# Kernel tuning notes

Measured on AMD Instinct MI355X. Metric: run time of the kernel, lower is better.

Reference implementation:

```python
import jax, jax.numpy as jnp
import numpy as np

NB, CH, NY, NX, NC = 2, 64, 80, 80, 80
STRIDE = 4.0


def _conv(x, w, b, pad):
    y = jax.lax.conv_general_dilated(x, w, (1, 1), [(pad, pad), (pad, pad)],
                                     dimension_numbers=('NCHW', 'OIHW', 'NCHW'))
    return y + b[None, :, None, None]


def _head(x, w1, b1, w2, b2, final_relu):
    y = jax.nn.relu(_conv(x, w1, b1, 1))
    y = _conv(y, w2, b2, 0)
    return jax.nn.relu(y) if final_relu else y


def setup_inputs() -> dict:
    key = jax.random.key(0)
    ks = jax.random.split(key, 16)
    s = 0.05

    def cw(k, o, i, kk):
        return jax.random.normal(k, (o, i, kk, kk), jnp.float32) * s

    def cb(k, o):
        return jax.random.normal(k, (o,), jnp.float32) * s

    inp = {
        'x': jax.random.normal(ks[0], (NB, CH, NY, NX), jnp.float32),
        # offsets: [batch_index, off_x, off_y] per image (esod tile offsets)
        'offsets': jnp.concatenate([
            jnp.arange(NB, dtype=jnp.float32)[:, None],
            jax.random.uniform(ks[1], (NB, 2), jnp.float32) * 4.0], axis=1),
        'hm_w1': cw(ks[2], CH, CH, 3), 'hm_b1': cb(ks[3], CH),
        'hm_w2': cw(ks[4], NC, CH, 1), 'hm_b2': jnp.full((NC,), -2.19, jnp.float32),
        'wh_w1': cw(ks[5], CH, CH, 3), 'wh_b1': cb(ks[6], CH),
        'wh_w2': cw(ks[7], 2, CH, 1), 'wh_b2': cb(ks[8], 2),
        'reg_w1': cw(ks[9], CH, CH, 3), 'reg_b1': cb(ks[10], CH),
        'reg_w2': cw(ks[11], 2, CH, 1), 'reg_b2': cb(ks[12], 2),
    }
    return inp


def _forward(x, offsets, hm_w1, hm_b1, hm_w2, hm_b2,
             wh_w1, wh_b1, wh_w2, wh_b2,
             reg_w1, reg_b1, reg_w2, reg_b2):
    hm = _head(x, hm_w1, hm_b1, hm_w2, hm_b2, False)    # (nb, nc, ny, nx)
    wh = _head(x, wh_w1, wh_b1, wh_w2, wh_b2, True)     # (nb, 2, ny, nx)
    reg = _head(x, reg_w1, reg_b1, reg_w2, reg_b2, True)
    nb, nc, ny, nx = hm.shape

    wh_ = jnp.transpose(wh, (0, 2, 3, 1))   # (nb, ny, nx, 2)
    reg_ = jnp.transpose(reg, (0, 2, 3, 1))
    yv, xv = jnp.meshgrid(jnp.arange(ny), jnp.arange(nx), indexing='ij')
    grid = jnp.stack([xv, yv], -1).astype(jnp.float32)[None]  # (1, ny, nx, 2)

    off_xy = offsets[:, 1:3].reshape(nb, 1, 1, 2) * 2.0
    ctr = grid + off_xy + reg_
    bbox = jnp.concatenate([ctr - wh_ / 2.0, ctr + wh_ / 2.0], -1) * STRIDE  # xyxy

    # xyxy -> xywh (same per-image boxes for every class channel)
    cxy = (bbox[..., :2] + bbox[..., 2:]) / 2.0
    bwh = bbox[..., 2:] - bbox[..., :2]
    xywh = jnp.concatenate([cxy, bwh], -1)              # (nb, ny, nx, 4)

    hm_ = jax.nn.sigmoid(hm)
    hmax = jax.lax.reduce_window(hm_, -jnp.inf, jax.lax.max,
                                 (1, 1, 3, 3), (1, 1, 1, 1),
                                 [(0, 0), (0, 0), (1, 1), (1, 1)])
    maxima = (hmax == hm_)                              # (nb, nc, ny, nx)

    no = 5 + nc
    xywh_b = jnp.broadcast_to(xywh[:, None], (nb, nc, ny, nx, 4))
    score = hm_[..., None]
    oh = jnp.broadcast_to(jnp.eye(nc, dtype=hm_.dtype)[None, :, None, None, :],
                          (nb, nc, ny, nx, nc))
    rows = jnp.concatenate([xywh_b, score, oh], -1)     # (nb, nc, ny, nx, no)

    K = nc * ny * nx
    rows = rows.reshape(nb, K, no)
    m = maxima.reshape(nb, K)

    def compact(r, mk):
        # stable sort: maxima rows first, preserving (c, y, x) scan order
        order = jnp.argsort(jnp.logical_not(mk), stable=True)
        return r[order] * mk[order][:, None].astype(r.dtype)

    return jax.vmap(compact)(rows, m)                   # (nb, K, 5+nc), zero-padded


def reference(x, offsets, hm_w1, hm_b1, hm_w2, hm_b2,
              wh_w1, wh_b1, wh_w2, wh_b2,
              reg_w1, reg_b1, reg_w2, reg_b2):
    return _forward(x, offsets, hm_w1, hm_b1, hm_w2, hm_b2,
                    wh_w1, wh_b1, wh_w2, wh_b2,
                    reg_w1, reg_b1, reg_w2, reg_b2)
```

## Files before the change

kernel.cpp:

```cpp
#include <hip/hip_runtime.h>
#include <math.h>

#define NBATCH 2
#define CHN    64
#define NYY    80
#define NXX    80
#define NCLS   80
#define NPIX   6400
#define KTOT   512000
#define NOUT   85
#define NBLK   500

typedef float vf4 __attribute__((ext_vector_type(4)));

#define QTOT   21760000L
#define QF1    13056000L
#define QF2    16320000L

__global__ __launch_bounds__(320)
void conv1_kernel(const float* __restrict__ x,
                  const float* __restrict__ hw1, const float* __restrict__ hb1,
                  const float* __restrict__ ww1, const float* __restrict__ wb1,
                  const float* __restrict__ rw1, const float* __restrict__ rb1,
                  double* __restrict__ c1hm, float* __restrict__ c1wr,
                  vf4* __restrict__ outq)
{
    __shared__ double smem_d[4992];
    const int bl = blockIdx.x;
    const int t  = threadIdx.x;

    const int gtid = bl * 320 + t;
    const int nth  = 640 * 320;
    const vf4 fz = {0.f, 0.f, 0.f, 0.f};

    if (bl < 320) {
        float*  lxf = (float*)smem_d;
        double* lwd = (double*)((char*)smem_d + 21504);

        const int yt  = bl % 40;
        const int ocg = (bl / 40) % 4;
        const int b   = bl / 160;

        const int pxq = t % 80;
        const int ocq = t / 80;
        const int r   = pxq / 40;
        const int c   = (pxq % 40) * 2;
        const int oc0 = ocg * 16 + ocq * 4;
        const int gy0 = yt * 2;

        const float* xin = x + (size_t)b * CHN * NPIX;

        double acc[2][4];
        #pragma unroll
        for (int j = 0; j < 2; j++)
            #pragma unroll
            for (int o = 0; o < 4; o++) acc[j][o] = (double)hb1[oc0 + o];

        for (int cc = 0; cc < 4; cc++) {
            const int icc = cc * 16;
            __syncthreads();
            for (int j = t; j < 1280; j += 320) {
                int ic_l = j / 80; int rem = j % 80;
                int row_l = rem / 20; int c4 = (rem % 20) * 4;
                int gy = gy0 - 1 + row_l;
                float4 v = make_float4(0.f, 0.f, 0.f, 0.f);
                if ((unsigned)gy < 80u)
                    v = *(const float4*)(xin + (size_t)(icc + ic_l) * NPIX + gy * NXX + c4);
                float* dst = &lxf[(ic_l * 4 + row_l) * 84];
                dst[c4 + 1] = v.x; dst[c4 + 2] = v.y;
                dst[c4 + 3] = v.z; dst[c4 + 4] = v.w;
            }
            for (int j = t; j < 64; j += 320) {
                lxf[j * 84 + 0]  = 0.f;
                lxf[j * 84 + 81] = 0.f;
            }
            for (int j = t; j < 2304; j += 320) {
                int oc_l = j % 16; int k = j / 16;
                int ic_l = k / 9, tap = k % 9;
                lwd[k * 16 + oc_l] =
                    (double)hw1[((size_t)(ocg * 16 + oc_l) * CHN + icc + ic_l) * 9 + tap];
            }
            __syncthreads();
            {
                int i0 = cc * 16, i1 = i0 + 16;
                for (int i = i0; i < i1; i++) {
                    long q = (long)gtid + (long)i * nth;
                    if (q < QF1) __builtin_nontemporal_store(fz, outq + q);
                }
            }
            for (int ic = 0; ic < 16; ic++) {
                double xw[3][4];
                #pragma unroll
                for (int ky = 0; ky < 3; ky++) {
                    const float* row = &lxf[(ic * 4 + r + ky) * 84];
                    float2 a  = *(const float2*)&row[c];
                    float2 bb = *(const float2*)&row[c + 2];
                    xw[ky][0] = (double)a.x;  xw[ky][1] = (double)a.y;
                    xw[ky][2] = (double)bb.x; xw[ky][3] = (double)bb.y;
                }
                #pragma unroll
                for (int ky = 0; ky < 3; ky++)
                #pragma unroll
                for (int kx = 0; kx < 3; kx++) {
                    const double* wv = &lwd[(ic * 9 + ky * 3 + kx) * 16 + ocq * 4];
                    double w0 = wv[0], w1d = wv[1], w2 = wv[2], w3 = wv[3];
                    double x0 = xw[ky][kx], x1 = xw[ky][kx + 1];
                    acc[0][0] += x0 * w0; acc[0][1] += x0 * w1d;
                    acc[0][2] += x0 * w2; acc[0][3] += x0 * w3;
                    acc[1][0] += x1 * w0; acc[1][1] += x1 * w1d;
                    acc[1][2] += x1 * w2; acc[1][3] += x1 * w3;
                }
            }
        }
        size_t pix = (size_t)(gy0 + r) * NXX + c;
        #pragma unroll
        for (int o = 0; o < 4; o++) {
            double2 v;
            v.x = acc[0][o] > 0.0 ? acc[0][o] : 0.0;
            v.y = acc[1][o] > 0.0 ? acc[1][o] : 0.0;
            *(double2*)(c1hm + ((size_t)b * CHN + oc0 + o) * NPIX + pix) = v;
        }
    } else {
        float* lxw = (float*)smem_d;
        float* lwf = (float*)((char*)smem_d + 30720);

        const int blw = bl - 320;
        const int yt  = blw % 20;
        const int ocg = (blw / 20) % 4;
        const int img = blw / 80;

        const int head = img >> 1, b = img & 1;
        const float* w1 = (head == 0) ? ww1 : rw1;
        const float* b1 = (head == 0) ? wb1 : rb1;
        const float* xin = x + (size_t)b * CHN * NPIX;

        const int pxq = t % 80;
        const int ocq = t / 80;
        const int r   = pxq / 20;
        const int c   = (pxq % 20) * 4;
        const int oc0 = ocg * 16 + ocq * 4;
        const int gy0 = yt * 4;

        float acc[4][4];
        #pragma unroll
        for (int j = 0; j < 4; j++)
            #pragma unroll
            for (int o = 0; o < 4; o++) acc[j][o] = b1[oc0 + o];

        for (int cc = 0; cc < 4; cc++) {
            const int icc = cc * 16;
            __syncthreads();
            for (int j = t; j < 1920; j += 320) {
                int ic_l = j / 120; int rem = j % 120;
                int row_l = rem / 20; int c4 = (rem % 20) * 4;
                int gy = gy0 - 1 + row_l;
                float4 v = make_float4(0.f, 0.f, 0.f, 0.f);
                if ((unsigned)gy < 80u)
                    v = *(const float4*)(xin + (size_t)(icc + ic_l) * NPIX + gy * NXX + c4);
                *(float4*)&lxw[(ic_l * 6 + row_l) * 80 + c4] = v;
            }
            for (int j = t; j < 2304; j += 320) {
                int oc_l = j % 16; int k = j / 16;
                int ic_l = k / 9, tap = k % 9;
                lwf[k * 16 + oc_l] =
                    w1[((size_t)(ocg * 16 + oc_l) * CHN + icc + ic_l) * 9 + tap];
            }
            __syncthreads();
            {
                int i0 = cc * 16, i1 = i0 + 16;
                for (int i = i0; i < i1; i++) {
                    long q = (long)gtid + (long)i * nth;
                    if (q < QF1) __builtin_nontemporal_store(fz, outq + q);
                }
            }
            for (int ic = 0; ic < 16; ic++) {
                float xw[3][6];
                #pragma unroll
                for (int ky = 0; ky < 3; ky++) {
                    const float* row = &lxw[(ic * 6 + r + ky) * 80];
                    xw[ky][0] = (c > 0) ? row[c - 1] : 0.f;
                    float4 m = *(const float4*)&row[c];
                    xw[ky][1] = m.x; xw[ky][2] = m.y;
                    xw[ky][3] = m.z; xw[ky][4] = m.w;
                    xw[ky][5] = (c < 76) ? row[c + 4] : 0.f;
                }
                #pragma unroll
                for (int ky = 0; ky < 3; ky++)
                #pragma unroll
                for (int kx = 0; kx < 3; kx++) {
                    const float* wv = &lwf[(ic * 9 + ky * 3 + kx) * 16 + ocq * 4];
                    float w0 = wv[0], w1v = wv[1], w2 = wv[2], w3 = wv[3];
                    #pragma unroll
                    for (int j = 0; j < 4; j++) {
                        float xv = xw[ky][j + kx];
                        acc[j][0] += xv * w0; acc[j][1] += xv * w1v;
                        acc[j][2] += xv * w2; acc[j][3] += xv * w3;
                    }
                }
            }
        }
        size_t pix = (size_t)(gy0 + r) * NXX + c;
        #pragma unroll
        for (int o = 0; o < 4; o++) {
            float4 v;
            v.x = fmaxf(acc[0][o], 0.f); v.y = fmaxf(acc[1][o], 0.f);
            v.z = fmaxf(acc[2][o], 0.f); v.w = fmaxf(acc[3][o], 0.f);
            *(float4*)(c1wr + ((size_t)img * CHN + oc0 + o) * NPIX + pix) = v;
        }
    }
}

__global__ __launch_bounds__(256)
void conv2_hm_kernel(const double* __restrict__ c1,
                     const float* __restrict__ w2,
                     const float* __restrict__ b2,
                     double* __restrict__ hm_z,
                     vf4* __restrict__ outq)
{
    int p   = blockIdx.x * 256 + threadIdx.x;
    int oc0 = blockIdx.y * 4;
    int b   = blockIdx.z;

    {
        const int bl   = (blockIdx.z * 20 + blockIdx.y) * 25 + blockIdx.x;
        const int gtid = bl * 256 + threadIdx.x;
        const vf4 fz = {0.f, 0.f, 0.f, 0.f};
        for (int i = 0; i < 13; i++) {
            long q = QF1 + (long)gtid + (long)i * 256000;
            if (q < QF2) __builtin_nontemporal_store(fz, outq + q);
        }
    }

    const double* in = c1 + (size_t)b * CHN * NPIX;
    double acc[4];
    #pragma unroll
    for (int o = 0; o < 4; o++) acc[o] = (double)b2[oc0 + o];

    for (int ic = 0; ic < CHN; ic++) {
        double xv = in[(size_t)ic * NPIX + p];
        #pragma unroll
        for (int o = 0; o < 4; o++)
            acc[o] += xv * (double)w2[(size_t)(oc0 + o) * CHN + ic];
    }
    #pragma unroll
    for (int o = 0; o < 4; o++)
        hm_z[((size_t)b * NCLS + oc0 + o) * NPIX + p] = acc[o];
}

__global__ __launch_bounds__(256)
void conv2_wr_kernel(const float* __restrict__ c1,
                     const float* __restrict__ wh_w2, const float* __restrict__ wh_b2,
                     const float* __restrict__ rg_w2, const float* __restrict__ rg_b2,
                     float* __restrict__ wh, float* __restrict__ rg)
{
    int p  = blockIdx.x * 256 + threadIdx.x;
    int hc = blockIdx.y;
    int b  = blockIdx.z;
    int head = hc >> 1, ch = hc & 1;

    const float* in = c1 + ((size_t)(head * 2 + b) * CHN) * NPIX;
    const float* w  = (head == 0) ? wh_w2 + (size_t)ch * CHN : rg_w2 + (size_t)ch * CHN;
    float bias      = (head == 0) ? wh_b2[ch] : rg_b2[ch];

    float acc = bias;
    for (int ic = 0; ic < CHN; ic++) acc += in[(size_t)ic * NPIX + p] * w[ic];
    acc = fmaxf(acc, 0.f);
    float* o = (head == 0) ? wh : rg;
    o[((size_t)b * 2 + ch) * NPIX + p] = acc;
}

__global__ void flags_kernel(const double* __restrict__ hm_z,
                             unsigned long long* __restrict__ ballots,
                             unsigned int* __restrict__ counts,
                             vf4* __restrict__ outq)
{
    int b = blockIdx.y;
    int k = blockIdx.x * 1024 + threadIdx.x;

    {
        const int gtid = (b * NBLK + blockIdx.x) * 1024 + threadIdx.x;
        const vf4 fz = {0.f, 0.f, 0.f, 0.f};
        for (int i = 0; i < 6; i++) {
            long q = QF2 + (long)gtid + (long)i * 1024000;
            if (q < QTOT) __builtin_nontemporal_store(fz, outq + q);
        }
    }

    int c = k / NPIX;
    int p = k - c * NPIX;
    int y = p / NXX, xx = p - y * NXX;

    const double* h = hm_z + ((size_t)b * NCLS + c) * NPIX;
    double s = h[p];
    double m = s;
    #pragma unroll
    for (int dy = -1; dy <= 1; dy++) {
        int yy = y + dy;
        if ((unsigned)yy >= (unsigned)NYY) continue;
        const double* hr = h + yy * NXX;
        #pragma unroll
        for (int dx = -1; dx <= 1; dx++) {
            int xn = xx + dx;
            if ((unsigned)xn >= (unsigned)NXX) continue;
            double v = hr[xn];
            m = v > m ? v : m;
        }
    }
    bool flag = (s == m);
    unsigned long long ball = __ballot(flag);
    int lane = threadIdx.x & 63;
    int wave = threadIdx.x >> 6;

    __shared__ unsigned int wcnt[16];
    if (lane == 0) {
        ballots[(size_t)b * 8000 + blockIdx.x * 16 + wave] = ball;
        wcnt[wave] = __popcll(ball);
    }
    __syncthreads();
    if (threadIdx.x == 0) {
        unsigned int tot = 0;
        for (int i = 0; i < 16; i++) tot += wcnt[i];
        counts[b * NBLK + blockIdx.x] = tot;
    }
}

__global__ void scan_kernel(const unsigned int* __restrict__ counts,
                            unsigned int* __restrict__ offs)
{
    int b = blockIdx.x;
    int t = threadIdx.x;
    unsigned int v = (t < NBLK) ? counts[b * NBLK + t] : 0u;
    unsigned int xi = v;
    #pragma unroll
    for (int d = 1; d < 64; d <<= 1) {
        unsigned int n = __shfl_up(xi, d, 64);
        if ((t & 63) >= d) xi += n;
    }
    __shared__ unsigned int wtot[8];
    __shared__ unsigned int wbase[8];
    if ((t & 63) == 63) wtot[t >> 6] = xi;
    __syncthreads();
    if (t == 0) {
        unsigned int a = 0;
        for (int i = 0; i < 8; i++) { wbase[i] = a; a += wtot[i]; }
    }
    __syncthreads();
    unsigned int excl = xi - v + wbase[t >> 6];
    if (t < NBLK) offs[b * NBLK + t] = excl;
}

__global__ void scatter_kernel(const unsigned long long* __restrict__ ballots,
                               const unsigned int* __restrict__ offs,
                               const double* __restrict__ hm_z,
                               const float* __restrict__ wh,
                               const float* __restrict__ rg,
                               const float* __restrict__ offsets,
                               float* __restrict__ out)
{
    int b = blockIdx.y;
    int k = blockIdx.x * 1024 + threadIdx.x;
    int lane = threadIdx.x & 63;
    int wave = threadIdx.x >> 6;

    unsigned long long ball = ballots[(size_t)b * 8000 + blockIdx.x * 16 + wave];

    __shared__ unsigned int wc[16];
    __shared__ unsigned int wb[16];
    if (lane == 0) wc[wave] = __popcll(ball);
    __syncthreads();
    if (threadIdx.x == 0) {
        unsigned int a = 0;
        for (int i = 0; i < 16; i++) { wb[i] = a; a += wc[i]; }
    }
    __syncthreads();

    bool flag = (ball >> lane) & 1ull;
    if (!flag) return;

    unsigned int rank = offs[b * NBLK + blockIdx.x] + wb[wave]
                      + (unsigned int)__popcll(ball & ((1ull << lane) - 1ull));

    int c = k / NPIX;
    int p = k - c * NPIX;
    int y = p / NXX, xx = p - y * NXX;

    float offx = offsets[b * 3 + 1];
    float offy = offsets[b * 3 + 2];
    float r0 = rg[((size_t)b * 2 + 0) * NPIX + p];
    float r1 = rg[((size_t)b * 2 + 1) * NPIX + p];
    float w0 = wh[((size_t)b * 2 + 0) * NPIX + p];
    float w1 = wh[((size_t)b * 2 + 1) * NPIX + p];
    double z = hm_z[((size_t)b * NCLS + c) * NPIX + p];
    float s  = (float)(1.0 / (1.0 + exp(-z)));

    float cx = ((float)xx + 2.f * offx + r0) * 4.f;
    float cy = ((float)y  + 2.f * offy + r1) * 4.f;

    float* row = out + ((size_t)b * KTOT + rank) * NOUT;
    row[0] = cx;
    row[1] = cy;
    row[2] = w0 * 4.f;
    row[3] = w1 * 4.f;
    row[4] = s;
    row[5 + c] = 1.f;
}

extern "C" void kernel_launch(void* const* d_in, const int* in_sizes, int n_in,
                              void* d_out, int out_size, void* d_ws, size_t ws_size,
                              hipStream_t stream)
{
    const float* x       = (const float*)d_in[0];
    const float* offsets = (const float*)d_in[1];
    const float* hm_w1   = (const float*)d_in[2];
    const float* hm_b1   = (const float*)d_in[3];
    const float* hm_w2   = (const float*)d_in[4];
    const float* hm_b2   = (const float*)d_in[5];
    const float* wh_w1   = (const float*)d_in[6];
    const float* wh_b1   = (const float*)d_in[7];
    const float* wh_w2   = (const float*)d_in[8];
    const float* wh_b2   = (const float*)d_in[9];
    const float* reg_w1  = (const float*)d_in[10];
    const float* reg_b1  = (const float*)d_in[11];
    const float* reg_w2  = (const float*)d_in[12];
    const float* reg_b2  = (const float*)d_in[13];

    float* out = (float*)d_out;
    vf4* outq  = (vf4*)d_out;

    char* wp = (char*)d_ws;
    double* c1hm = (double*)wp;                 wp += (size_t)NBATCH * CHN * NPIX * 8;
    double* hm_z = (double*)wp;                 wp += (size_t)NBATCH * NCLS * NPIX * 8;
    float*  c1wr = (float*)wp;                  wp += (size_t)2 * NBATCH * CHN * NPIX * 4;
    float*  wh   = (float*)wp;                  wp += (size_t)NBATCH * 2 * NPIX * 4;
    float*  rg   = (float*)wp;                  wp += (size_t)NBATCH * 2 * NPIX * 4;
    unsigned long long* ballots = (unsigned long long*)wp; wp += (size_t)NBATCH * 8000 * 8;
    unsigned int* counts = (unsigned int*)wp;   wp += (size_t)NBATCH * NBLK * 4;
    unsigned int* offs   = (unsigned int*)wp;

    conv1_kernel<<<640, 320, 0, stream>>>(
        x, hm_w1, hm_b1, wh_w1, wh_b1, reg_w1, reg_b1, c1hm, c1wr, outq);

    conv2_hm_kernel<<<dim3(25, 20, 2), 256, 0, stream>>>(c1hm, hm_w2, hm_b2, hm_z, outq);

    conv2_wr_kernel<<<dim3(25, 4, 2), 256, 0, stream>>>(
        c1wr, wh_w2, wh_b2, reg_w2, reg_b2, wh, rg);

    flags_kernel<<<dim3(NBLK, 2), 1024, 0, stream>>>(hm_z, ballots, counts, outq);

    scan_kernel<<<2, 512, 0, stream>>>(counts, offs);

    scatter_kernel<<<dim3(NBLK, 2), 1024, 0, stream>>>(
        ballots, offs, hm_z, wh, rg, offsets, out);
}
```

Before: 154.4 us.

## Double conv1 grid with smaller per-block tiles and rebalance output zeroing across kernels

Splits conv1 work into twice as many blocks: the fp64 heatmap path now computes 8 output channels per block instead of 16, and the wh/reg path uses 2-row tiles with a padded shared layout matching the hm path. Shared memory per block shrinks, which can raise occupancy. The zero-fill of the output buffer is redistributed: flags_kernel now zeroes fewer chunks and scatter_kernel zeroes the final region. The intent is more parallelism for conv1 and spreading memset traffic, at the cost of more redundant input loads and scatter blocks that both zero and write output.

```diff
diff --git a/kernel.cpp b/kernel.cpp
--- a/kernel.cpp
+++ b/kernel.cpp
@@ -16,6 +16,7 @@
 #define QTOT   21760000L
 #define QF1    13056000L
 #define QF2    16320000L
+#define QF3    19584000L
 
 __global__ __launch_bounds__(320)
 void conv1_kernel(const float* __restrict__ x,
@@ -25,36 +26,37 @@
                   double* __restrict__ c1hm, float* __restrict__ c1wr,
                   vf4* __restrict__ outq)
 {
-    __shared__ double smem_d[4992];
+    __shared__ double smem_d[3840];
     const int bl = blockIdx.x;
     const int t  = threadIdx.x;
 
     const int gtid = bl * 320 + t;
-    const int nth  = 640 * 320;
+    const int nth  = 1280 * 320;
     const vf4 fz = {0.f, 0.f, 0.f, 0.f};
 
-    if (bl < 320) {
-        float*  lxf = (float*)smem_d;
+    const int pxq = t % 80;
+    const int ocq = t / 80;
+    const int r   = pxq / 40;
+    const int c   = (pxq % 40) * 2;
+
+    float* lxf = (float*)smem_d;
+
+    if (bl < 640) {
         double* lwd = (double*)((char*)smem_d + 21504);
 
         const int yt  = bl % 40;
-        const int ocg = (bl / 40) % 4;
-        const int b   = bl / 160;
-
-        const int pxq = t % 80;
-        const int ocq = t / 80;
-        const int r   = pxq / 40;
-        const int c   = (pxq % 40) * 2;
-        const int oc0 = ocg * 16 + ocq * 4;
+        const int ocg = (bl / 40) % 8;
+        const int b   = bl / 320;
+        const int oc0 = ocg * 8 + ocq * 2;
         const int gy0 = yt * 2;
 
         const float* xin = x + (size_t)b * CHN * NPIX;
 
-        double acc[2][4];
+        double acc[2][2];
         #pragma unroll
         for (int j = 0; j < 2; j++)
             #pragma unroll
-            for (int o = 0; o < 4; o++) acc[j][o] = (double)hb1[oc0 + o];
+            for (int o = 0; o < 2; o++) acc[j][o] = (double)hb1[oc0 + o];
 
         for (int cc = 0; cc < 4; cc++) {
             const int icc = cc * 16;
@@ -74,15 +76,15 @@
                 lxf[j * 84 + 0]  = 0.f;
                 lxf[j * 84 + 81] = 0.f;
             }
-            for (int j = t; j < 2304; j += 320) {
-                int oc_l = j % 16; int k = j / 16;
+            for (int j = t; j < 1152; j += 320) {
+                int oc_l = j % 8; int k = j / 8;
                 int ic_l = k / 9, tap = k % 9;
-                lwd[k * 16 + oc_l] =
-                    (double)hw1[((size_t)(ocg * 16 + oc_l) * CHN + icc + ic_l) * 9 + tap];
+                lwd[k * 8 + oc_l] =
+                    (double)hw1[((size_t)(ocg * 8 + oc_l) * CHN + icc + ic_l) * 9 + tap];
             }
             __syncthreads();
             {
-                int i0 = cc * 16, i1 = i0 + 16;
+                int i0 = cc * 8, i1 = i0 + 8;
                 for (int i = i0; i < i1; i++) {
                     long q = (long)gtid + (long)i * nth;
                     if (q < QF1) __builtin_nontemporal_store(fz, outq + q);
@@ -102,62 +104,61 @@
                 for (int ky = 0; ky < 3; ky++)
                 #pragma unroll
                 for (int kx = 0; kx < 3; kx++) {
-                    const double* wv = &lwd[(ic * 9 + ky * 3 + kx) * 16 + ocq * 4];
-                    double w0 = wv[0], w1d = wv[1], w2 = wv[2], w3 = wv[3];
+                    const double* wv = &lwd[(ic * 9 + ky * 3 + kx) * 8 + ocq * 2];
+                    double w0 = wv[0], w1d = wv[1];
                     double x0 = xw[ky][kx], x1 = xw[ky][kx + 1];
                     acc[0][0] += x0 * w0; acc[0][1] += x0 * w1d;
-                    acc[0][2] += x0 * w2; acc[0][3] += x0 * w3;
                     acc[1][0] += x1 * w0; acc[1][1] += x1 * w1d;
-                    acc[1][2] += x1 * w2; acc[1][3] += x1 * w3;
-                }
-            }
-        }
-        size_t pix = (size_t)(gy0 + r) * NXX + c;
-        #pragma unroll
-        for (int o = 0; o < 4; o++) {
+                }
+            }
+        }
+        size_t pix = (size_t)((bl % 40) * 2 + r) * NXX + c;
+        #pragma unroll
+        for (int o = 0; o < 2; o++) {
             double2 v;
             v.x = acc[0][o] > 0.0 ? acc[0][o] : 0.0;
             v.y = acc[1][o] > 0.0 ? acc[1][o] : 0.0;
             *(double2*)(c1hm + ((size_t)b * CHN + oc0 + o) * NPIX + pix) = v;
         }
     } else {
-        float* lxw = (float*)smem_d;
-        float* lwf = (float*)((char*)smem_d + 30720);
-
-        const int blw = bl - 320;
-        const int yt  = blw % 20;
-        const int ocg = (blw / 20) % 4;
-        const int img = blw / 80;
+        float* lwf = (float*)((char*)smem_d + 21504);
+
+        const int blw = bl - 640;
+        const int yt  = blw % 40;
+        const int ocg = (blw / 40) % 4;
+        const int img = blw / 160;
 
         const int head = img >> 1, b = img & 1;
         const float* w1 = (head == 0) ? ww1 : rw1;
         const float* b1 = (head == 0) ? wb1 : rb1;
         const float* xin = x + (size_t)b * CHN * NPIX;
 
-        const int pxq = t % 80;
-        const int ocq = t / 80;
-        const int r   = pxq / 20;
-        const int c   = (pxq % 20) * 4;
         const int oc0 = ocg * 16 + ocq * 4;
-        const int gy0 = yt * 4;
-
-        float acc[4][4];
-        #pragma unroll
-        for (int j = 0; j < 4; j++)
+        const int gy0 = yt * 2;
+
+        float acc[2][4];
+        #pragma unroll
+        for (int j = 0; j < 2; j++)
             #pragma unroll
             for (int o = 0; o < 4; o++) acc[j][o] = b1[oc0 + o];
 
         for (int cc = 0; cc < 4; cc++) {
             const int icc = cc * 16;
             __syncthreads();
-            for (int j = t; j < 1920; j += 320) {
-                int ic_l = j / 120; int rem = j % 120;
+            for (int j = t; j < 1280; j += 320) {
+                int ic_l = j / 80; int rem = j % 80;
                 int row_l = rem / 20; int c4 = (rem % 20) * 4;
                 int gy = gy0 - 1 + row_l;
                 float4 v = make_float4(0.f, 0.f, 0.f, 0.f);
                 if ((unsigned)gy < 80u)
                     v = *(const float4*)(xin + (size_t)(icc + ic_l) * NPIX + gy * NXX + c4);
-                *(float4*)&lxw[(ic_l * 6 + row_l) * 80 + c4] = v;
+                float* dst = &lxf[(ic_l * 4 + row_l) * 84];
+                dst[c4 + 1] = v.x; dst[c4 + 2] = v.y;
+                dst[c4 + 3] = v.z; dst[c4 + 4] = v.w;
+            }
+            for (int j = t; j < 64; j += 320) {
+                lxf[j * 84 + 0]  = 0.f;
+                lxf[j * 84 + 81] = 0.f;
             }
             for (int j = t; j < 2304; j += 320) {
                 int oc_l = j % 16; int k = j / 16;
@@ -167,22 +168,21 @@
             }
             __syncthreads();
             {
-                int i0 = cc * 16, i1 = i0 + 16;
+                int i0 = cc * 8, i1 = i0 + 8;
                 for (int i = i0; i < i1; i++) {
                     long q = (long)gtid + (long)i * nth;
                     if (q < QF1) __builtin_nontemporal_store(fz, outq + q);
                 }
             }
             for (int ic = 0; ic < 16; ic++) {
-                float xw[3][6];
+                float xw[3][4];
                 #pragma unroll
                 for (int ky = 0; ky < 3; ky++) {
-                    const float* row = &lxw[(ic * 6 + r + ky) * 80];
-                    xw[ky][0] = (c > 0) ? row[c - 1] : 0.f;
-                    float4 m = *(const float4*)&row[c];
-                    xw[ky][1] = m.x; xw[ky][2] = m.y;
-                    xw[ky][3] = m.z; xw[ky][4] = m.w;
-                    xw[ky][5] = (c < 76) ? row[c + 4] : 0.f;
+                    const float* row = &lxf[(ic * 4 + r + ky) * 84];
+                    float2 a  = *(const float2*)&row[c];
+                    float2 bb = *(const float2*)&row[c + 2];
+                    xw[ky][0] = a.x;  xw[ky][1] = a.y;
+                    xw[ky][2] = bb.x; xw[ky][3] = bb.y;
                 }
                 #pragma unroll
                 for (int ky = 0; ky < 3; ky++)
@@ -190,22 +190,21 @@
                 for (int kx = 0; kx < 3; kx++) {
                     const float* wv = &lwf[(ic * 9 + ky * 3 + kx) * 16 + ocq * 4];
                     float w0 = wv[0], w1v = wv[1], w2 = wv[2], w3 = wv[3];
-                    #pragma unroll
-                    for (int j = 0; j < 4; j++) {
-                        float xv = xw[ky][j + kx];
-                        acc[j][0] += xv * w0; acc[j][1] += xv * w1v;
-                        acc[j][2] += xv * w2; acc[j][3] += xv * w3;
-                    }
+                    float x0 = xw[ky][kx], x1 = xw[ky][kx + 1];
+                    acc[0][0] += x0 * w0; acc[0][1] += x0 * w1v;
+                    acc[0][2] += x0 * w2; acc[0][3] += x0 * w3;
+                    acc[1][0] += x1 * w0; acc[1][1] += x1 * w1v;
+                    acc[1][2] += x1 * w2; acc[1][3] += x1 * w3;
                 }
             }
         }
         size_t pix = (size_t)(gy0 + r) * NXX + c;
         #pragma unroll
         for (int o = 0; o < 4; o++) {
-            float4 v;
-            v.x = fmaxf(acc[0][o], 0.f); v.y = fmaxf(acc[1][o], 0.f);
-            v.z = fmaxf(acc[2][o], 0.f); v.w = fmaxf(acc[3][o], 0.f);
-            *(float4*)(c1wr + ((size_t)img * CHN + oc0 + o) * NPIX + pix) = v;
+            float2 v;
+            v.x = fmaxf(acc[0][o], 0.f);
+            v.y = fmaxf(acc[1][o], 0.f);
+            *(float2*)(c1wr + ((size_t)img * CHN + oc0 + o) * NPIX + pix) = v;
         }
     }
 }
@@ -280,9 +279,9 @@
     {
         const int gtid = (b * NBLK + blockIdx.x) * 1024 + threadIdx.x;
         const vf4 fz = {0.f, 0.f, 0.f, 0.f};
-        for (int i = 0; i < 6; i++) {
+        for (int i = 0; i < 4; i++) {
             long q = QF2 + (long)gtid + (long)i * 1024000;
-            if (q < QTOT) __builtin_nontemporal_store(fz, outq + q);
+            if (q < QF3) __builtin_nontemporal_store(fz, outq + q);
         }
     }
 
@@ -355,12 +354,22 @@
                                const float* __restrict__ wh,
                                const float* __restrict__ rg,
                                const float* __restrict__ offsets,
-                               float* __restrict__ out)
+                               float* __restrict__ out,
+                               vf4* __restrict__ outq)
 {
     int b = blockIdx.y;
     int k = blockIdx.x * 1024 + threadIdx.x;
     int lane = threadIdx.x & 63;
     int wave = threadIdx.x >> 6;
+
+    {
+        const int gtid = (b * NBLK + blockIdx.x) * 1024 + threadIdx.x;
+        const vf4 fz = {0.f, 0.f, 0.f, 0.f};
+        for (int i = 0; i < 3; i++) {
+            long q = QF3 + (long)gtid + (long)i * 1024000;
+            if (q < QTOT) __builtin_nontemporal_store(fz, outq + q);
+        }
+    }
 
     unsigned long long ball = ballots[(size_t)b * 8000 + blockIdx.x * 16 + wave];
 
@@ -437,7 +446,7 @@
     unsigned int* counts = (unsigned int*)wp;   wp += (size_t)NBATCH * NBLK * 4;
     unsigned int* offs   = (unsigned int*)wp;
 
-    conv1_kernel<<<640, 320, 0, stream>>>(
+    conv1_kernel<<<1280, 320, 0, stream>>>(
         x, hm_w1, hm_b1, wh_w1, wh_b1, reg_w1, reg_b1, c1hm, c1wr, outq);
 
     conv2_hm_kernel<<<dim3(25, 20, 2), 256, 0, stream>>>(c1hm, hm_w2, hm_b2, hm_z, outq);
@@ -450,5 +459,5 @@
     scan_kernel<<<2, 512, 0, stream>>>(counts, offs);
 
     scatter_kernel<<<dim3(NBLK, 2), 1024, 0, stream>>>(
-        ballots, offs, hm_z, wh, rg, offsets, out);
-}
+        ballots, offs, hm_z, wh, rg, offsets, out, outq);
+}
```

Measured after the change: 190.7 us. +23.6%, slower.

## Fuse hm/wh/reg 1x1 convs with 3x3 maxpool flagging in one kernel

Applied to the files above, without the earlier changes.

Merges the heatmap 1x1 conv, the wh/reg 1x1 convs and the local-maximum flag computation into a single kernel. Each block computes a 4-row tile plus halo rows of heatmap logits for four classes, keeps them in shared memory and produces ballots and counts directly, so the separate flags pass no longer re-reads hm_z. Scan and scatter are reorganised around 80x4-pixel segments (1600 per image), and the output zero-fill work is redistributed between kernels. The cost is recomputing the halo rows (1.5x the heatmap conv work) and a longer scan.

```diff
diff --git a/kernel.cpp b/kernel.cpp
--- a/kernel.cpp
+++ b/kernel.cpp
@@ -9,13 +9,12 @@
 #define NPIX   6400
 #define KTOT   512000
 #define NOUT   85
-#define NBLK   500
 
 typedef float vf4 __attribute__((ext_vector_type(4)));
 
 #define QTOT   21760000L
 #define QF1    13056000L
-#define QF2    16320000L
+#define QF2    17856000L
 
 __global__ __launch_bounds__(320)
 void conv1_kernel(const float* __restrict__ x,
@@ -210,179 +209,208 @@
     }
 }
 
-__global__ __launch_bounds__(256)
-void conv2_hm_kernel(const double* __restrict__ c1,
-                     const float* __restrict__ w2,
-                     const float* __restrict__ b2,
-                     double* __restrict__ hm_z,
-                     vf4* __restrict__ outq)
+__global__ __launch_bounds__(320)
+void conv2_kernel(const double* __restrict__ c1hm,
+                  const float* __restrict__ hm_w2, const float* __restrict__ hm_b2,
+                  const float* __restrict__ c1wr,
+                  const float* __restrict__ wh_w2, const float* __restrict__ wh_b2,
+                  const float* __restrict__ rg_w2, const float* __restrict__ rg_b2,
+                  double* __restrict__ hm_z, float* __restrict__ wh, float* __restrict__ rg,
+                  unsigned long long* __restrict__ ballots,
+                  unsigned int* __restrict__ counts,
+                  vf4* __restrict__ outq)
 {
-    int p   = blockIdx.x * 256 + threadIdx.x;
-    int oc0 = blockIdx.y * 4;
-    int b   = blockIdx.z;
+    __shared__ double lz[4][6][80];
+    __shared__ double lw[64][4];
+    __shared__ unsigned int wcnt[4][5];
+
+    const int bl = blockIdx.x;
+    const int t  = threadIdx.x;
 
     {
-        const int bl   = (blockIdx.z * 20 + blockIdx.y) * 25 + blockIdx.x;
-        const int gtid = bl * 256 + threadIdx.x;
+        const int gtid = bl * 320 + t;
         const vf4 fz = {0.f, 0.f, 0.f, 0.f};
-        for (int i = 0; i < 13; i++) {
-            long q = QF1 + (long)gtid + (long)i * 256000;
+        for (int i = 0; i < 16; i++) {
+            long q = QF1 + (long)gtid + (long)i * 307200;
             if (q < QF2) __builtin_nontemporal_store(fz, outq + q);
         }
     }
 
-    const double* in = c1 + (size_t)b * CHN * NPIX;
-    double acc[4];
-    #pragma unroll
-    for (int o = 0; o < 4; o++) acc[o] = (double)b2[oc0 + o];
-
-    for (int ic = 0; ic < CHN; ic++) {
-        double xv = in[(size_t)ic * NPIX + p];
-        #pragma unroll
-        for (int o = 0; o < 4; o++)
-            acc[o] += xv * (double)w2[(size_t)(oc0 + o) * CHN + ic];
-    }
-    #pragma unroll
-    for (int o = 0; o < 4; o++)
-        hm_z[((size_t)b * NCLS + oc0 + o) * NPIX + p] = acc[o];
+    if (bl < 800) {
+        const int rt = bl % 20;
+        const int cg = (bl / 20) % 20;
+        const int b  = bl / 400;
+        const int y0 = rt * 4;
+
+        if (t < 256) {
+            int ic = t & 63, o = t >> 6;
+            lw[ic][o] = (double)hm_w2[(size_t)(cg * 4 + o) * CHN + ic];
+        }
+        __syncthreads();
+
+        const double* in = c1hm + (size_t)b * CHN * NPIX;
+        double bias[4];
+        #pragma unroll
+        for (int o = 0; o < 4; o++) bias[o] = (double)hm_b2[cg * 4 + o];
+
+        for (int j = t; j < 480; j += 320) {
+            int jr = j / 80, px = j % 80;
+            int gy = y0 - 1 + jr;
+            double z0 = -1.0e300, z1 = -1.0e300, z2 = -1.0e300, z3 = -1.0e300;
+            if ((unsigned)gy < 80u) {
+                int p = gy * 80 + px;
+                double a0 = bias[0], a1 = bias[1], a2 = bias[2], a3 = bias[3];
+                for (int ic = 0; ic < CHN; ic++) {
+                    double xv = in[(size_t)ic * NPIX + p];
+                    a0 += xv * lw[ic][0]; a1 += xv * lw[ic][1];
+                    a2 += xv * lw[ic][2]; a3 += xv * lw[ic][3];
+                }
+                z0 = a0; z1 = a1; z2 = a2; z3 = a3;
+                if (jr >= 1 && jr <= 4) {
+                    hm_z[((size_t)b * NCLS + cg * 4 + 0) * NPIX + p] = z0;
+                    hm_z[((size_t)b * NCLS + cg * 4 + 1) * NPIX + p] = z1;
+                    hm_z[((size_t)b * NCLS + cg * 4 + 2) * NPIX + p] = z2;
+                    hm_z[((size_t)b * NCLS + cg * 4 + 3) * NPIX + p] = z3;
+                }
+            }
+            lz[0][jr][px] = z0; lz[1][jr][px] = z1;
+            lz[2][jr][px] = z2; lz[3][jr][px] = z3;
+        }
+        __syncthreads();
+
+        const int wave = t >> 6, lane = t & 63;
+        const int idx = wave * 64 + lane;
+        const int ry = idx / 80, px = idx % 80;
+        #pragma unroll
+        for (int o = 0; o < 4; o++) {
+            double s = lz[o][ry + 1][px];
+            double m = s;
+            #pragma unroll
+            for (int dy = -1; dy <= 1; dy++) {
+                const double* row = &lz[o][ry + 1 + dy][0];
+                #pragma unroll
+                for (int dx = -1; dx <= 1; dx++) {
+                    int xn = px + dx;
+                    if ((unsigned)xn < 80u) {
+                        double v = row[xn];
+                        m = v > m ? v : m;
+                    }
+                }
+            }
+            bool flag = (s == m);
+            unsigned long long ball = __ballot(flag);
+            if (lane == 0) {
+                int c = cg * 4 + o;
+                ballots[(size_t)b * 8000 + c * 100 + rt * 5 + wave] = ball;
+                wcnt[o][wave] = __popcll(ball);
+            }
+        }
+        __syncthreads();
+        if (t < 4) {
+            unsigned int tot = 0;
+            #pragma unroll
+            for (int w = 0; w < 5; w++) tot += wcnt[t][w];
+            counts[b * 1600 + (cg * 4 + t) * 20 + rt] = tot;
+        }
+    } else {
+        const int blw  = bl - 800;
+        const int chunk = blw % 20;
+        const int hc   = (blw / 20) % 4;
+        const int b    = blw / 80;
+        const int head = hc >> 1, ch = hc & 1;
+
+        const int p = chunk * 320 + t;
+        const float* in = c1wr + ((size_t)(head * 2 + b) * CHN) * NPIX;
+        const float* w  = (head == 0) ? wh_w2 + (size_t)ch * CHN : rg_w2 + (size_t)ch * CHN;
+        float acc = (head == 0) ? wh_b2[ch] : rg_b2[ch];
+        for (int ic = 0; ic < CHN; ic++) acc += in[(size_t)ic * NPIX + p] * w[ic];
+        acc = fmaxf(acc, 0.f);
+        float* o = (head == 0) ? wh : rg;
+        o[((size_t)b * 2 + ch) * NPIX + p] = acc;
+    }
 }
 
-__global__ __launch_bounds__(256)
-void conv2_wr_kernel(const float* __restrict__ c1,
-                     const float* __restrict__ wh_w2, const float* __restrict__ wh_b2,
-                     const float* __restrict__ rg_w2, const float* __restrict__ rg_b2,
-                     float* __restrict__ wh, float* __restrict__ rg)
-{
-    int p  = blockIdx.x * 256 + threadIdx.x;
-    int hc = blockIdx.y;
-    int b  = blockIdx.z;
-    int head = hc >> 1, ch = hc & 1;
-
-    const float* in = c1 + ((size_t)(head * 2 + b) * CHN) * NPIX;
-    const float* w  = (head == 0) ? wh_w2 + (size_t)ch * CHN : rg_w2 + (size_t)ch * CHN;
-    float bias      = (head == 0) ? wh_b2[ch] : rg_b2[ch];
-
-    float acc = bias;
-    for (int ic = 0; ic < CHN; ic++) acc += in[(size_t)ic * NPIX + p] * w[ic];
-    acc = fmaxf(acc, 0.f);
-    float* o = (head == 0) ? wh : rg;
-    o[((size_t)b * 2 + ch) * NPIX + p] = acc;
-}
-
-__global__ void flags_kernel(const double* __restrict__ hm_z,
-                             unsigned long long* __restrict__ ballots,
-                             unsigned int* __restrict__ counts,
-                             vf4* __restrict__ outq)
-{
-    int b = blockIdx.y;
-    int k = blockIdx.x * 1024 + threadIdx.x;
-
-    {
-        const int gtid = (b * NBLK + blockIdx.x) * 1024 + threadIdx.x;
-        const vf4 fz = {0.f, 0.f, 0.f, 0.f};
-        for (int i = 0; i < 6; i++) {
-            long q = QF2 + (long)gtid + (long)i * 1024000;
-            if (q < QTOT) __builtin_nontemporal_store(fz, outq + q);
-        }
-    }
-
-    int c = k / NPIX;
-    int p = k - c * NPIX;
-    int y = p / NXX, xx = p - y * NXX;
-
-    const double* h = hm_z + ((size_t)b * NCLS + c) * NPIX;
-    double s = h[p];
-    double m = s;
-    #pragma unroll
-    for (int dy = -1; dy <= 1; dy++) {
-        int yy = y + dy;
-        if ((unsigned)yy >= (unsigned)NYY) continue;
-        const double* hr = h + yy * NXX;
-        #pragma unroll
-        for (int dx = -1; dx <= 1; dx++) {
-            int xn = xx + dx;
-            if ((unsigned)xn >= (unsigned)NXX) continue;
-            double v = hr[xn];
-            m = v > m ? v : m;
-        }
-    }
-    bool flag = (s == m);
-    unsigned long long ball = __ballot(flag);
-    int lane = threadIdx.x & 63;
-    int wave = threadIdx.x >> 6;
-
-    __shared__ unsigned int wcnt[16];
-    if (lane == 0) {
-        ballots[(size_t)b * 8000 + blockIdx.x * 16 + wave] = ball;
-        wcnt[wave] = __popcll(ball);
-    }
-    __syncthreads();
-    if (threadIdx.x == 0) {
-        unsigned int tot = 0;
-        for (int i = 0; i < 16; i++) tot += wcnt[i];
-        counts[b * NBLK + blockIdx.x] = tot;
-    }
-}
-
-__global__ void scan_kernel(const unsigned int* __restrict__ counts,
-                            unsigned int* __restrict__ offs)
+__global__ __launch_bounds__(1024)
+void scan_kernel(const unsigned int* __restrict__ counts,
+                 unsigned int* __restrict__ offs)
 {
     int b = blockIdx.x;
     int t = threadIdx.x;
-    unsigned int v = (t < NBLK) ? counts[b * NBLK + t] : 0u;
-    unsigned int xi = v;
+    int i0 = 2 * t, i1 = 2 * t + 1;
+    unsigned int e0 = (i0 < 1600) ? counts[b * 1600 + i0] : 0u;
+    unsigned int e1 = (i1 < 1600) ? counts[b * 1600 + i1] : 0u;
+    unsigned int s = e0 + e1;
+    unsigned int xi = s;
     #pragma unroll
     for (int d = 1; d < 64; d <<= 1) {
         unsigned int n = __shfl_up(xi, d, 64);
         if ((t & 63) >= d) xi += n;
     }
-    __shared__ unsigned int wtot[8];
-    __shared__ unsigned int wbase[8];
+    __shared__ unsigned int wtot[16];
+    __shared__ unsigned int wbase[16];
     if ((t & 63) == 63) wtot[t >> 6] = xi;
     __syncthreads();
     if (t == 0) {
         unsigned int a = 0;
-        for (int i = 0; i < 8; i++) { wbase[i] = a; a += wtot[i]; }
+        for (int i = 0; i < 16; i++) { wbase[i] = a; a += wtot[i]; }
     }
     __syncthreads();
-    unsigned int excl = xi - v + wbase[t >> 6];
-    if (t < NBLK) offs[b * NBLK + t] = excl;
+    unsigned int excl = xi - s + wbase[t >> 6];
+    if (i0 < 1600) offs[b * 1600 + i0] = excl;
+    if (i1 < 1600) offs[b * 1600 + i1] = excl + e0;
 }
 
-__global__ void scatter_kernel(const unsigned long long* __restrict__ ballots,
-                               const unsigned int* __restrict__ offs,
-                               const double* __restrict__ hm_z,
-                               const float* __restrict__ wh,
-                               const float* __restrict__ rg,
-                               const float* __restrict__ offsets,
-                               float* __restrict__ out)
+__global__ __launch_bounds__(320)
+void scatter_kernel(const unsigned long long* __restrict__ ballots,
+                    const unsigned int* __restrict__ offs,
+                    const double* __restrict__ hm_z,
+                    const float* __restrict__ wh,
+                    const float* __restrict__ rg,
+                    const float* __restrict__ offsets,
+                    float* __restrict__ out,
+                    vf4* __restrict__ outq)
 {
-    int b = blockIdx.y;
-    int k = blockIdx.x * 1024 + threadIdx.x;
-    int lane = threadIdx.x & 63;
-    int wave = threadIdx.x >> 6;
-
-    unsigned long long ball = ballots[(size_t)b * 8000 + blockIdx.x * 16 + wave];
-
-    __shared__ unsigned int wc[16];
-    __shared__ unsigned int wb[16];
-    if (lane == 0) wc[wave] = __popcll(ball);
+    __shared__ unsigned long long lball[5];
+    __shared__ unsigned int pre[5];
+
+    const int seg = blockIdx.x;
+    const int b   = blockIdx.y;
+    const int t   = threadIdx.x;
+    const int c   = seg / 20, rt = seg % 20;
+
+    {
+        const int gtid = (b * 1600 + seg) * 320 + t;
+        const vf4 fz = {0.f, 0.f, 0.f, 0.f};
+        for (int i = 0; i < 4; i++) {
+            long q = QF2 + (long)gtid + (long)i * 1024000;
+            if (q < QTOT) __builtin_nontemporal_store(fz, outq + q);
+        }
+    }
+
+    if (t < 5) {
+        unsigned long long ball = ballots[(size_t)b * 8000 + c * 100 + rt * 5 + t];
+        lball[t] = ball;
+        pre[t] = __popcll(ball);
+    }
     __syncthreads();
-    if (threadIdx.x == 0) {
-        unsigned int a = 0;
-        for (int i = 0; i < 16; i++) { wb[i] = a; a += wc[i]; }
+    if (t == 0) {
+        unsigned int run = offs[b * 1600 + seg];
+        #pragma unroll
+        for (int i = 0; i < 5; i++) { unsigned int v = pre[i]; pre[i] = run; run += v; }
     }
     __syncthreads();
 
-    bool flag = (ball >> lane) & 1ull;
-    if (!flag) return;
-
-    unsigned int rank = offs[b * NBLK + blockIdx.x] + wb[wave]
+    const int wave = t >> 6, lane = t & 63;
+    unsigned long long ball = lball[wave];
+    if (!((ball >> lane) & 1ull)) return;
+
+    unsigned int rank = pre[wave]
                       + (unsigned int)__popcll(ball & ((1ull << lane) - 1ull));
 
-    int c = k / NPIX;
-    int p = k - c * NPIX;
-    int y = p / NXX, xx = p - y * NXX;
+    const int idx = wave * 64 + lane;
+    const int y = rt * 4 + idx / 80;
+    const int xx = idx % 80;
+    const int p = y * 80 + xx;
 
     float offx = offsets[b * 3 + 1];
     float offy = offsets[b * 3 + 2];
@@ -434,21 +462,18 @@
     float*  wh   = (float*)wp;                  wp += (size_t)NBATCH * 2 * NPIX * 4;
     float*  rg   = (float*)wp;                  wp += (size_t)NBATCH * 2 * NPIX * 4;
     unsigned long long* ballots = (unsigned long long*)wp; wp += (size_t)NBATCH * 8000 * 8;
-    unsigned int* counts = (unsigned int*)wp;   wp += (size_t)NBATCH * NBLK * 4;
+    unsigned int* counts = (unsigned int*)wp;   wp += (size_t)NBATCH * 1600 * 4;
     unsigned int* offs   = (unsigned int*)wp;
 
     conv1_kernel<<<640, 320, 0, stream>>>(
         x, hm_w1, hm_b1, wh_w1, wh_b1, reg_w1, reg_b1, c1hm, c1wr, outq);
 
-    conv2_hm_kernel<<<dim3(25, 20, 2), 256, 0, stream>>>(c1hm, hm_w2, hm_b2, hm_z, outq);
-
-    conv2_wr_kernel<<<dim3(25, 4, 2), 256, 0, stream>>>(
-        c1wr, wh_w2, wh_b2, reg_w2, reg_b2, wh, rg);
-
-    flags_kernel<<<dim3(NBLK, 2), 1024, 0, stream>>>(hm_z, ballots, counts, outq);
-
-    scan_kernel<<<2, 512, 0, stream>>>(counts, offs);
-
-    scatter_kernel<<<dim3(NBLK, 2), 1024, 0, stream>>>(
-        ballots, offs, hm_z, wh, rg, offsets, out);
+    conv2_kernel<<<960, 320, 0, stream>>>(
+        c1hm, hm_w2, hm_b2, c1wr, wh_w2, wh_b2, reg_w2, reg_b2,
+        hm_z, wh, rg, ballots, counts, outq);
+
+    scan_kernel<<<2, 1024, 0, stream>>>(counts, offs);
+
+    scatter_kernel<<<dim3(1600, 2), 320, 0, stream>>>(
+        ballots, offs, hm_z, wh, rg, offsets, out, outq);
 }
```

After: 414.3 us. 2.68x slower.

## Tile hm 1x1 conv in shared memory and rebalance output zero-fill across kernels

Applied to the files above, without the earlier changes.

The heatmap 1x1 conv now runs as 200 blocks. Each block stages a 64-pixel by 64-channel input tile and the full 64x80 weight matrix in LDS as doubles, and each thread accumulates 20 output channels. This raises reuse of inputs and weights compared with the old 4-outputs-per-thread layout, which reread the input once per 4 channels. The zero-fill of the large output is also redistributed: less in conv2_hm (fewer blocks), some in flags, and a new slice in scatter. The 72KB of LDS per block and 20 double accumulators per thread lower occupancy, and a fill now shares time with the scatter's own writes.

```diff
diff --git a/kernel.cpp b/kernel.cpp
--- a/kernel.cpp
+++ b/kernel.cpp
@@ -15,7 +15,8 @@
 
 #define QTOT   21760000L
 #define QF1    13056000L
-#define QF2    16320000L
+#define QF2    13721600L
+#define QF3    19584000L
 
 __global__ __launch_bounds__(320)
 void conv1_kernel(const float* __restrict__ x,
@@ -217,34 +218,49 @@
                      double* __restrict__ hm_z,
                      vf4* __restrict__ outq)
 {
-    int p   = blockIdx.x * 256 + threadIdx.x;
-    int oc0 = blockIdx.y * 4;
-    int b   = blockIdx.z;
+    __shared__ double lx[64 * 64];
+    __shared__ double lw[64 * 80];
+
+    const int bl  = blockIdx.x;
+    const int t   = threadIdx.x;
+    const int b   = bl / 100;
+    const int px0 = (bl % 100) * 64;
 
     {
-        const int bl   = (blockIdx.z * 20 + blockIdx.y) * 25 + blockIdx.x;
-        const int gtid = bl * 256 + threadIdx.x;
+        const int gtid = bl * 256 + t;
         const vf4 fz = {0.f, 0.f, 0.f, 0.f};
         for (int i = 0; i < 13; i++) {
-            long q = QF1 + (long)gtid + (long)i * 256000;
+            long q = QF1 + (long)gtid + (long)i * 51200;
             if (q < QF2) __builtin_nontemporal_store(fz, outq + q);
         }
     }
 
     const double* in = c1 + (size_t)b * CHN * NPIX;
-    double acc[4];
+    for (int j = t; j < 4096; j += 256) {
+        int ic = j >> 6, px = j & 63;
+        lx[j] = in[(size_t)ic * NPIX + px0 + px];
+    }
+    for (int j = t; j < 5120; j += 256) {
+        int ic = j / 80, oc = j % 80;
+        lw[j] = (double)w2[(size_t)oc * CHN + ic];
+    }
+    __syncthreads();
+
+    const int px  = t & 63;
+    const int ocg = t >> 6;
+    double acc[20];
     #pragma unroll
-    for (int o = 0; o < 4; o++) acc[o] = (double)b2[oc0 + o];
-
-    for (int ic = 0; ic < CHN; ic++) {
-        double xv = in[(size_t)ic * NPIX + p];
-        #pragma unroll
-        for (int o = 0; o < 4; o++)
-            acc[o] += xv * (double)w2[(size_t)(oc0 + o) * CHN + ic];
+    for (int o = 0; o < 20; o++) acc[o] = (double)b2[ocg * 20 + o];
+
+    for (int ic = 0; ic < 64; ic++) {
+        double xv = lx[ic * 64 + px];
+        const double* wrow = &lw[ic * 80 + ocg * 20];
+        #pragma unroll
+        for (int o = 0; o < 20; o++) acc[o] += xv * wrow[o];
     }
     #pragma unroll
-    for (int o = 0; o < 4; o++)
-        hm_z[((size_t)b * NCLS + oc0 + o) * NPIX + p] = acc[o];
+    for (int o = 0; o < 20; o++)
+        hm_z[((size_t)b * NCLS + ocg * 20 + o) * NPIX + px0 + px] = acc[o];
 }
 
 __global__ __launch_bounds__(256)
@@ -282,7 +298,7 @@
         const vf4 fz = {0.f, 0.f, 0.f, 0.f};
         for (int i = 0; i < 6; i++) {
             long q = QF2 + (long)gtid + (long)i * 1024000;
-            if (q < QTOT) __builtin_nontemporal_store(fz, outq + q);
+            if (q < QF3) __builtin_nontemporal_store(fz, outq + q);
         }
     }
 
@@ -355,12 +371,22 @@
                                const float* __restrict__ wh,
                                const float* __restrict__ rg,
                                const float* __restrict__ offsets,
-                               float* __restrict__ out)
+                               float* __restrict__ out,
+                               vf4* __restrict__ outq)
 {
     int b = blockIdx.y;
     int k = blockIdx.x * 1024 + threadIdx.x;
     int lane = threadIdx.x & 63;
     int wave = threadIdx.x >> 6;
+
+    {
+        const int gtid = (b * NBLK + blockIdx.x) * 1024 + threadIdx.x;
+        const vf4 fz = {0.f, 0.f, 0.f, 0.f};
+        for (int i = 0; i < 3; i++) {
+            long q = QF3 + (long)gtid + (long)i * 1024000;
+            if (q < QTOT) __builtin_nontemporal_store(fz, outq + q);
+        }
+    }
 
     unsigned long long ball = ballots[(size_t)b * 8000 + blockIdx.x * 16 + wave];
 
@@ -440,7 +466,7 @@
     conv1_kernel<<<640, 320, 0, stream>>>(
         x, hm_w1, hm_b1, wh_w1, wh_b1, reg_w1, reg_b1, c1hm, c1wr, outq);
 
-    conv2_hm_kernel<<<dim3(25, 20, 2), 256, 0, stream>>>(c1hm, hm_w2, hm_b2, hm_z, outq);
+    conv2_hm_kernel<<<200, 256, 0, stream>>>(c1hm, hm_w2, hm_b2, hm_z, outq);
 
     conv2_wr_kernel<<<dim3(25, 4, 2), 256, 0, stream>>>(
         c1wr, wh_w2, wh_b2, reg_w2, reg_b2, wh, rg);
@@ -450,5 +476,5 @@
     scan_kernel<<<2, 512, 0, stream>>>(counts, offs);
 
     scatter_kernel<<<dim3(NBLK, 2), 1024, 0, stream>>>(
-        ballots, offs, hm_z, wh, rg, offsets, out);
-}
+        ballots, offs, hm_z, wh, rg, offsets, out, outq);
+}
```

Result: slower. 158.6 us (+2.8%).
